# Optimization experiments

Measured on AMD Instinct MI355X. Metric: run time of the kernel, lower is better.

Reference implementation:

```python
import jax, jax.numpy as jnp
import numpy as np

NUM_HEAD = 8
GN_GROUPS = 32
EPS = 1e-5


def group_norm(x, w, b):
    # x: [B,C,H,W]; GroupNorm over 32 groups
    B, C, H, W = x.shape
    xg = x.reshape(B, GN_GROUPS, C // GN_GROUPS, H, W)
    mu = jnp.mean(xg, axis=(2, 3, 4), keepdims=True)
    var = jnp.var(xg, axis=(2, 3, 4), keepdims=True)
    xn = ((xg - mu) * jax.lax.rsqrt(var + EPS)).reshape(B, C, H, W)
    return xn * w[None, :, None, None] + b[None, :, None, None]


def conv1x1(x, w, b):
    # 1x1 conv == channel-wise linear: w [O,C], x [B,C,H,W]
    return jnp.einsum('oc,bchw->bohw', w, x) + b[None, :, None, None]


def setup_inputs() -> dict:
    key = jax.random.key(0)
    ks = jax.random.split(key, 6)
    B, C, H, W = 8, 512, 32, 32
    s = 1.0 / np.sqrt(C)
    return {
        'x': jax.random.normal(ks[0], (B, C, H, W), jnp.float32),
        'gn_w': jnp.ones((C,), jnp.float32),
        'gn_b': jnp.zeros((C,), jnp.float32),
        'wq': jax.random.normal(ks[1], (C, C), jnp.float32) * s,
        'bq': jnp.zeros((C,), jnp.float32),
        'wk': jax.random.normal(ks[2], (C, C), jnp.float32) * s,
        'bk': jnp.zeros((C,), jnp.float32),
        'wv': jax.random.normal(ks[3], (C, C), jnp.float32) * s,
        'bv': jnp.zeros((C,), jnp.float32),
        'wo': jax.random.normal(ks[4], (C, C), jnp.float32) * s,
        'bo': jnp.zeros((C,), jnp.float32),
    }


def reference(x, gn_w, gn_b, wq, bq, wk, bk, wv, bv, wo, bo):
    B, C, H, W = x.shape
    Hn = NUM_HEAD
    d = C // Hn
    N = H * W
    scale = d ** -0.5

    xn = group_norm(x, gn_w, gn_b)
    q = conv1x1(xn, wq, bq).reshape(B, Hn, d, N)  # [B,Hn,d,N]
    k = conv1x1(xn, wk, bk).reshape(B, Hn, d, N)
    v = conv1x1(xn, wv, bv).reshape(B, Hn, d, N)

    # attn[b,h,i,j] = sum_d q[b,h,d,i] * k[b,h,d,j]
    attn = jnp.einsum('bhdi,bhdj->bhij', q, k) * scale
    attn = jax.nn.softmax(attn, axis=-1)
    # out[b,h,d,i] = sum_j attn[b,h,i,j] * v[b,h,d,j]
    out = jnp.einsum('bhij,bhdj->bhdi', attn, v).reshape(B, C, H, W)
    return x + conv1x1(out, wo, bo)
```

## Files before the change

### kernel.cpp

```cpp
#include <hip/hip_runtime.h>
#include <hip/hip_bf16.h>

typedef unsigned short ushort_t;
typedef __bf16 bf16_t;
typedef bf16_t bf16x8 __attribute__((ext_vector_type(8)));
typedef float f32x4 __attribute__((ext_vector_type(4)));
typedef float f32x16 __attribute__((ext_vector_type(16)));

#define CH 512
#define NSP 1024

__device__ __forceinline__ float bf2f(ushort_t u) {
    union { unsigned int i; float f; } t; t.i = ((unsigned int)u) << 16; return t.f;
}
__device__ __forceinline__ ushort_t f2bf(float f) {
    union { float fl; unsigned int i; } t; t.fl = f;
    unsigned int r = t.i + 0x7fffu + ((t.i >> 16) & 1u);
    return (ushort_t)(r >> 16);
}
__device__ __forceinline__ unsigned int pk2(float a, float b) {
    __hip_bfloat162 h = __float22bfloat162_rn(make_float2(a, b));
    union { __hip_bfloat162 h2; unsigned int u; } t; t.h2 = h; return t.u;
}

#if __has_builtin(__builtin_amdgcn_global_load_lds)
#define HAVE_ASYNC_LDS 1
#endif
__device__ __forceinline__ void cp16(const ushort_t* g, ushort_t* l) {
#ifdef HAVE_ASYNC_LDS
    __builtin_amdgcn_global_load_lds((const __attribute__((address_space(1))) unsigned int*)g,
                                     (__attribute__((address_space(3))) unsigned int*)l, 16, 0, 0);
#else
    *(uint4*)l = *(const uint4*)g;
#endif
}

#if __has_builtin(__builtin_amdgcn_exp2f)
#define EXP2(x) __builtin_amdgcn_exp2f(x)
#else
#define EXP2(x) exp2f(x)
#endif

#define QSCALE 0.18033688011112042f

__global__ __launch_bounds__(256) void prep_gn(const float* __restrict__ x, const float* __restrict__ gw,
                                               const float* __restrict__ gbias,
                                               const float* __restrict__ w0, const float* __restrict__ w1,
                                               const float* __restrict__ w2, const float* __restrict__ w3,
                                               ushort_t* __restrict__ wbf, ushort_t* __restrict__ xnt) {
    int tid = threadIdx.x;
    if (blockIdx.x >= 256) {
        int idx = (blockIdx.x - 256) * 256 + tid;
        int my = idx >> 16;
        const float* src = (my == 0) ? w0 : (my == 1) ? w1 : (my == 2) ? w2 : w3;
        float4 v = reinterpret_cast<const float4*>(src)[idx & 65535];
        uint2 u = make_uint2(pk2(v.x, v.y), pk2(v.z, v.w));
        reinterpret_cast<uint2*>(wbf + (size_t)my * 262144)[idx & 65535] = u;
        return;
    }
    __shared__ float red[8];
    int bg = blockIdx.x;
    int b = bg >> 5, g = bg & 31;
    const float4* x4 = reinterpret_cast<const float4*>(x + (size_t)bg * 16384);
    float4 v[16];
    float s = 0.f, s2 = 0.f;
    #pragma unroll
    for (int i = 0; i < 16; i++) {
        v[i] = x4[i * 256 + tid];
        s  += v[i].x + v[i].y + v[i].z + v[i].w;
        s2 += v[i].x * v[i].x + v[i].y * v[i].y + v[i].z * v[i].z + v[i].w * v[i].w;
    }
    #pragma unroll
    for (int off = 32; off > 0; off >>= 1) {
        s  += __shfl_down(s, off, 64);
        s2 += __shfl_down(s2, off, 64);
    }
    int wv = tid >> 6;
    if ((tid & 63) == 0) { red[wv] = s; red[4 + wv] = s2; }
    __syncthreads();
    float ts  = red[0] + red[1] + red[2] + red[3];
    float ts2 = red[4] + red[5] + red[6] + red[7];
    float mu  = ts * (1.f / 16384.f);
    float var = ts2 * (1.f / 16384.f) - mu * mu;
    float rstd = rsqrtf(var + 1e-5f);
    float ca[16], cb[16];
    #pragma unroll
    for (int cc = 0; cc < 16; cc++) {
        float ww = gw[g * 16 + cc], bb = gbias[g * 16 + cc];
        ca[cc] = rstd * ww; cb[cc] = bb - mu * ca[cc];
    }
    #pragma unroll
    for (int jj = 0; jj < 4; jj++) {
        float e[16];
        #pragma unroll
        for (int cc = 0; cc < 16; cc++) {
            float xv = (jj == 0) ? v[cc].x : (jj == 1) ? v[cc].y : (jj == 2) ? v[cc].z : v[cc].w;
            e[cc] = xv * ca[cc] + cb[cc];
        }
        uint4 u0 = make_uint4(pk2(e[0], e[1]), pk2(e[2], e[3]), pk2(e[4], e[5]), pk2(e[6], e[7]));
        uint4 u1 = make_uint4(pk2(e[8], e[9]), pk2(e[10], e[11]), pk2(e[12], e[13]), pk2(e[14], e[15]));
        ushort_t* dst = xnt + ((size_t)(b * 1024 + 4 * tid + jj)) * 512 + g * 16;
        *reinterpret_cast<uint4*>(dst)     = u0;
        *reinterpret_cast<uint4*>(dst + 8) = u1;
    }
}

__global__ __launch_bounds__(256) void conv_qkv(const ushort_t* __restrict__ xnt,
                                                const ushort_t* __restrict__ wbf,
                                                const float* __restrict__ bq,
                                                const float* __restrict__ bk,
                                                const float* __restrict__ bv,
                                                ushort_t* __restrict__ qt,
                                                ushort_t* __restrict__ kt,
                                                ushort_t* __restrict__ vt) {
    __shared__ __align__(16) char smem[17408];
    ushort_t* als = (ushort_t*)smem;
    ushort_t* bls = (ushort_t*)(smem + 8192);
    int tid = threadIdx.x;
    int wave = tid >> 6, lane = tid & 63, l15 = lane & 15, quad = lane >> 4;
    int wm = wave >> 1, wn = wave & 1;
    int m0 = blockIdx.x * 128, o0 = blockIdx.y * 64, b = blockIdx.z;
    const ushort_t* A = xnt + (size_t)b * 524288;

    f32x4 acc[4][2];
    #pragma unroll
    for (int ms = 0; ms < 4; ms++)
        #pragma unroll
        for (int ns = 0; ns < 2; ns++) acc[ms][ns] = (f32x4){0.f, 0.f, 0.f, 0.f};

    for (int k0 = 0; k0 < 512; k0 += 32) {
        #pragma unroll
        for (int rep = 0; rep < 2; rep++) {
            int id = rep * 256 + tid;
            int r = id >> 2, part = id & 3;
            int sw = part ^ ((r >> 2) & 3);
            cp16(A + (size_t)(m0 + r) * 512 + k0 + sw * 8, als + (size_t)id * 8);
        }
        {
            int r = tid >> 2, part = tid & 3;
            int sw = part ^ ((r >> 2) & 3);
            cp16(wbf + (size_t)(o0 + r) * 512 + k0 + sw * 8, bls + (size_t)tid * 8);
        }
        __syncthreads();
        bf16x8 af[4], bfr[2];
        #pragma unroll
        for (int ms = 0; ms < 4; ms++) {
            int row = wm * 64 + ms * 16 + l15;
            int slot = quad ^ ((row >> 2) & 3);
            af[ms] = *(const bf16x8*)(als + row * 32 + slot * 8);
        }
        #pragma unroll
        for (int ns = 0; ns < 2; ns++) {
            int row = wn * 32 + ns * 16 + l15;
            int slot = quad ^ ((row >> 2) & 3);
            bfr[ns] = *(const bf16x8*)(bls + row * 32 + slot * 8);
        }
        #pragma unroll
        for (int ms = 0; ms < 4; ms++)
            #pragma unroll
            for (int ns = 0; ns < 2; ns++)
                acc[ms][ns] = __builtin_amdgcn_mfma_f32_16x16x32_bf16(af[ms], bfr[ns], acc[ms][ns], 0, 0, 0);
        __syncthreads();
    }

    int seg = o0 >> 9, lo = o0 & 511;
    if (seg < 2) {
        const float* bias = seg ? bk : bq;
        ushort_t* dst = seg ? kt : qt;
        float s = seg ? 1.f : QSCALE;
        float bv0 = bias[lo + wn * 32 + l15];
        float bv1 = bias[lo + wn * 32 + 16 + l15];
        ushort_t* cls = (ushort_t*)smem;
        #pragma unroll
        for (int ms = 0; ms < 4; ms++)
            #pragma unroll
            for (int ns = 0; ns < 2; ns++) {
                float bb = ns ? bv1 : bv0;
                int idx = (wm * 64 + ms * 16 + quad * 4) * 64 + wn * 32 + ns * 16 + l15;
                unsigned int ua = pk2((acc[ms][ns][0] + bb) * s, (acc[ms][ns][1] + bb) * s);
                unsigned int ub = pk2((acc[ms][ns][2] + bb) * s, (acc[ms][ns][3] + bb) * s);
                cls[idx]       = (ushort_t)(ua & 0xffff);
                cls[idx + 64]  = (ushort_t)(ua >> 16);
                cls[idx + 128] = (ushort_t)(ub & 0xffff);
                cls[idx + 192] = (ushort_t)(ub >> 16);
            }
        __syncthreads();
        int h = lo >> 6;
        size_t obase = ((size_t)(b * 8 + h) * 1024 + m0) * 64;
        #pragma unroll
        for (int rep = 0; rep < 4; rep++) {
            int id = rep * 256 + tid;
            int r = id >> 3, part = id & 7;
            *(uint4*)(dst + obase + (size_t)r * 64 + part * 8) = *(const uint4*)(cls + r * 64 + part * 8);
        }
    } else {
        float bv0 = bv[lo + wn * 32 + l15];
        float bv1 = bv[lo + wn * 32 + 16 + l15];
        ushort_t* clst = (ushort_t*)smem;
        #pragma unroll
        for (int ms = 0; ms < 4; ms++)
            #pragma unroll
            for (int ns = 0; ns < 2; ns++) {
                float bb = ns ? bv1 : bv0;
                unsigned int ua = pk2(acc[ms][ns][0] + bb, acc[ms][ns][1] + bb);
                unsigned int ub = pk2(acc[ms][ns][2] + bb, acc[ms][ns][3] + bb);
                *(uint2*)(&clst[(wn * 32 + ns * 16 + l15) * 136 + wm * 64 + ms * 16 + quad * 4]) =
                    make_uint2(ua, ub);
            }
        __syncthreads();
        #pragma unroll
        for (int rep = 0; rep < 4; rep++) {
            int id = rep * 256 + tid;
            int row = id >> 4, part = id & 15;
            *(uint4*)(vt + ((size_t)(b * 512 + lo + row) * 1024 + m0 + part * 8)) =
                *(const uint4*)(clst + row * 136 + part * 8);
        }
    }
}

#define Z16 {0.f,0.f,0.f,0.f,0.f,0.f,0.f,0.f,0.f,0.f,0.f,0.f,0.f,0.f,0.f,0.f}

#define PV_STEP(JS, P) {                                                                     \
    unsigned wA0 = pk2(P[((JS)&1)*8+0], P[((JS)&1)*8+1]);                                    \
    unsigned wA1 = pk2(P[((JS)&1)*8+2], P[((JS)&1)*8+3]);                                    \
    unsigned wB0 = pk2(P[((JS)&1)*8+4], P[((JS)&1)*8+5]);                                    \
    unsigned wB1 = pk2(P[((JS)&1)*8+6], P[((JS)&1)*8+7]);                                    \
    asm("v_permlane32_swap_b32 %0, %1" : "+v"(wA0), "+v"(wB0));                              \
    asm("v_permlane32_swap_b32 %0, %1" : "+v"(wA1), "+v"(wB1));                              \
    union { unsigned u[4]; bf16x8 v; } pa_;                                                  \
    pa_.u[0] = wA0; pa_.u[1] = wA1; pa_.u[2] = wB0; pa_.u[3] = wB1;                          \
    int phys_ = (((JS) * 2) | hi) ^ r7;                                                      \
    bf16x8 vf0 = *(const bf16x8*)(vbuf + l31 * 64 + phys_ * 8);                              \
    bf16x8 vf1 = *(const bf16x8*)(vbuf + (32 + l31) * 64 + phys_ * 8);                       \
    __builtin_amdgcn_s_setprio(1);                                                           \
    vacc0 = __builtin_amdgcn_mfma_f32_32x32x16_bf16(pa_.v, vf0, vacc0, 0, 0, 0);             \
    vacc1 = __builtin_amdgcn_mfma_f32_32x32x16_bf16(pa_.v, vf1, vacc1, 0, 0, 0);             \
    __builtin_amdgcn_s_setprio(0); }

__global__ __launch_bounds__(256) void attn_kernel(const ushort_t* __restrict__ qt,
                                                   const ushort_t* __restrict__ kt,
                                                   const ushort_t* __restrict__ vt,
                                                   ushort_t* __restrict__ ao) {
    __shared__ __align__(16) ushort_t smem[24576];
    int tid = threadIdx.x;
    int wave = tid >> 6, lane = tid & 63, l31 = lane & 31, hi = lane >> 5;
    int id = blockIdx.x;
    int bh = (id & 7) * 8 + (id >> 6);
    int i0 = ((id >> 3) & 7) * 128;
    const ushort_t* qb = qt + (size_t)bh * 65536;
    const ushort_t* kb = kt + (size_t)bh * 65536;
    const ushort_t* vb = vt + (size_t)bh * 65536;
    int iw0 = i0 + wave * 32;
    int r7 = l31 & 7;

    bf16x8 qf[4];
    #pragma unroll
    for (int ks = 0; ks < 4; ks++)
        qf[ks] = *(const bf16x8*)(qb + (size_t)(iw0 + l31) * 64 + ks * 16 + hi * 8);

    f32x16 vacc0 = Z16, vacc1 = Z16;
    float lacc = 0.f;

    int rk0 = tid >> 3, sk = tid & 7, rk1 = rk0 + 32;
    const ushort_t* kg0 = kb + rk0 * 64 + (sk ^ (rk0 & 7)) * 8;
    const ushort_t* kg1 = kb + rk1 * 64 + (sk ^ (rk1 & 7)) * 8;
    const ushort_t* vg0 = vb + (size_t)rk0 * 1024 + (sk ^ (rk0 & 7)) * 8;
    const ushort_t* vg1 = vb + (size_t)rk1 * 1024 + (sk ^ (rk1 & 7)) * 8;

    cp16(kg0, smem + tid * 8);
    cp16(kg1, smem + (tid + 256) * 8);
    cp16(vg0, smem + 12288 + tid * 8);
    cp16(vg1, smem + 12288 + (tid + 256) * 8);
    kg0 += 4096; kg1 += 4096; vg0 += 64; vg1 += 64;
    cp16(kg0, smem + 4096 + tid * 8);
    cp16(kg1, smem + 4096 + (tid + 256) * 8);
    cp16(vg0, smem + 16384 + tid * 8);
    cp16(vg1, smem + 16384 + (tid + 256) * 8);
    kg0 += 4096; kg1 += 4096; vg0 += 64; vg1 += 64;

    for (int jt = 0; jt < 16; jt++) {
        if (jt == 15) asm volatile("s_waitcnt vmcnt(0)" ::: "memory");
        else          asm volatile("s_waitcnt vmcnt(4)" ::: "memory");
        __builtin_amdgcn_s_barrier();
        __builtin_amdgcn_sched_barrier(0);
        if (jt < 14) {
            int nb = jt + 2 - ((jt + 2) >= 3 ? 3 : 0) - ((jt + 2) >= 6 ? 3 : 0)
                     - ((jt + 2) >= 9 ? 3 : 0) - ((jt + 2) >= 12 ? 3 : 0) - ((jt + 2) >= 15 ? 3 : 0);
            ushort_t* kd = smem + nb * 4096;
            ushort_t* vd = smem + 12288 + nb * 4096;
            cp16(kg0, kd + tid * 8);
            cp16(kg1, kd + (tid + 256) * 8);
            cp16(vg0, vd + tid * 8);
            cp16(vg1, vd + (tid + 256) * 8);
            kg0 += 4096; kg1 += 4096; vg0 += 64; vg1 += 64;
        }
        int cur = jt - (jt >= 3 ? 3 : 0) - (jt >= 6 ? 3 : 0) - (jt >= 9 ? 3 : 0)
                  - (jt >= 12 ? 3 : 0) - (jt >= 15 ? 3 : 0);
        const ushort_t* kbuf = smem + cur * 4096;
        const ushort_t* vbuf = smem + 12288 + cur * 4096;

        f32x16 s0 = Z16, s1 = Z16;
        __builtin_amdgcn_s_setprio(1);
        #pragma unroll
        for (int ks = 0; ks < 4; ks++) {
            int phys = ((ks * 2) | hi) ^ r7;
            bf16x8 kf = *(const bf16x8*)(kbuf + l31 * 64 + phys * 8);
            s0 = __builtin_amdgcn_mfma_f32_32x32x16_bf16(kf, qf[ks], s0, 0, 0, 0);
        }
        #pragma unroll
        for (int ks = 0; ks < 4; ks++) {
            int phys = ((ks * 2) | hi) ^ r7;
            bf16x8 kf = *(const bf16x8*)(kbuf + (32 + l31) * 64 + phys * 8);
            s1 = __builtin_amdgcn_mfma_f32_32x32x16_bf16(kf, qf[ks], s1, 0, 0, 0);
        }
        __builtin_amdgcn_s_setprio(0);

        float p0[16], p1[16];
        #pragma unroll
        for (int r = 0; r < 16; r++) p0[r] = EXP2(s0[r]);
        #pragma unroll
        for (int r = 0; r < 16; r++) p1[r] = EXP2(s1[r]);
        float t0 = 0.f, t1 = 0.f, t2 = 0.f, t3 = 0.f;
        #pragma unroll
        for (int r = 0; r < 4; r++) { t0 += p0[r]; t1 += p0[4 + r]; t2 += p0[8 + r]; t3 += p0[12 + r]; }
        #pragma unroll
        for (int r = 0; r < 4; r++) { t0 += p1[r]; t1 += p1[4 + r]; t2 += p1[8 + r]; t3 += p1[12 + r]; }
        lacc += (t0 + t1) + (t2 + t3);

        PV_STEP(0, p0)
        PV_STEP(1, p0)
        PV_STEP(2, p1)
        PV_STEP(3, p1)
    }

    __syncthreads();

    lacc += __shfl_xor(lacc, 32, 64);
    float linv[16];
    #pragma unroll
    for (int r = 0; r < 16; r++) {
        int ir = (r & 3) + 8 * (r >> 2) + 4 * hi;
        linv[r] = 1.f / __shfl(lacc, ir, 64);
    }

    ushort_t* ols = smem;
    #pragma unroll
    for (int r = 0; r < 16; r++) {
        int irow = wave * 32 + (r & 3) + 8 * (r >> 2) + 4 * hi;
        ols[irow * 80 + l31]      = f2bf(vacc0[r] * linv[r]);
        ols[irow * 80 + 32 + l31] = f2bf(vacc1[r] * linv[r]);
    }
    __syncthreads();
    int b = bh >> 3, h = bh & 7;
    ushort_t* aob = ao + ((size_t)b * 1024 + i0) * 512 + h * 64;
    #pragma unroll
    for (int rep = 0; rep < 4; rep++) {
        int idd = rep * 256 + tid;
        int rl = idd >> 3, part = idd & 7;
        *(uint4*)(aob + (size_t)rl * 512 + part * 8) = *(const uint4*)(ols + rl * 80 + part * 8);
    }
}

__global__ __launch_bounds__(256) void conv_out(const ushort_t* __restrict__ ao,
                                                const ushort_t* __restrict__ wo,
                                                const float* __restrict__ bo,
                                                const float* __restrict__ xres,
                                                float* __restrict__ out) {
    __shared__ __align__(16) char smem[12288];
    ushort_t* als = (ushort_t*)smem;
    ushort_t* bls = (ushort_t*)(smem + 8192);
    int tid = threadIdx.x;
    int wave = tid >> 6, lane = tid & 63, l15 = lane & 15, quad = lane >> 4;
    int wm = wave >> 1, wn = wave & 1;
    int m0 = blockIdx.x * 128, o0 = blockIdx.y * 64, b = blockIdx.z;
    const ushort_t* A = ao + (size_t)b * 524288;

    f32x4 acc[4][2];
    #pragma unroll
    for (int ms = 0; ms < 4; ms++)
        #pragma unroll
        for (int ns = 0; ns < 2; ns++) acc[ms][ns] = (f32x4){0.f, 0.f, 0.f, 0.f};

    for (int k0 = 0; k0 < 512; k0 += 32) {
        #pragma unroll
        for (int rep = 0; rep < 2; rep++) {
            int id = rep * 256 + tid;
            int r = id >> 2, part = id & 3;
            int sw = part ^ ((r >> 2) & 3);
            cp16(A + (size_t)(m0 + r) * 512 + k0 + sw * 8, als + (size_t)id * 8);
        }
        {
            int r = tid >> 2, part = tid & 3;
            int sw = part ^ ((r >> 2) & 3);
            cp16(wo + (size_t)(o0 + r) * 512 + k0 + sw * 8, bls + (size_t)tid * 8);
        }
        __syncthreads();
        bf16x8 af[4], bfr[2];
        #pragma unroll
        for (int ms = 0; ms < 4; ms++) {
            int row = wm * 64 + ms * 16 + l15;
            int slot = quad ^ ((row >> 2) & 3);
            af[ms] = *(const bf16x8*)(als + row * 32 + slot * 8);
        }
        #pragma unroll
        for (int ns = 0; ns < 2; ns++) {
            int row = wn * 32 + ns * 16 + l15;
            int slot = quad ^ ((row >> 2) & 3);
            bfr[ns] = *(const bf16x8*)(bls + row * 32 + slot * 8);
        }
        #pragma unroll
        for (int ms = 0; ms < 4; ms++)
            #pragma unroll
            for (int ns = 0; ns < 2; ns++)
                acc[ms][ns] = __builtin_amdgcn_mfma_f32_16x16x32_bf16(af[ms], bfr[ns], acc[ms][ns], 0, 0, 0);
        __syncthreads();
    }

    #pragma unroll
    for (int ns = 0; ns < 2; ns++) {
        int o = o0 + wn * 32 + ns * 16 + l15;
        float bb = bo[o];
        #pragma unroll
        for (int ms = 0; ms < 4; ms++) {
            int n = m0 + wm * 64 + ms * 16 + quad * 4;
            size_t ga = ((size_t)(b * 512 + o)) * 1024 + n;
            float4 xv = *(const float4*)(xres + ga);
            float4 c4;
            c4.x = acc[ms][ns][0] + bb + xv.x;
            c4.y = acc[ms][ns][1] + bb + xv.y;
            c4.z = acc[ms][ns][2] + bb + xv.z;
            c4.w = acc[ms][ns][3] + bb + xv.w;
            *(float4*)(out + ga) = c4;
        }
    }
}

extern "C" void kernel_launch(void* const* d_in, const int* in_sizes, int n_in,
                              void* d_out, int out_size, void* d_ws, size_t ws_size,
                              hipStream_t stream) {
    const float* x    = (const float*)d_in[0];
    const float* gn_w = (const float*)d_in[1];
    const float* gn_b = (const float*)d_in[2];
    const float* wq   = (const float*)d_in[3];
    const float* bq   = (const float*)d_in[4];
    const float* wk   = (const float*)d_in[5];
    const float* bk   = (const float*)d_in[6];
    const float* wv   = (const float*)d_in[7];
    const float* bv   = (const float*)d_in[8];
    const float* wo   = (const float*)d_in[9];
    const float* bo   = (const float*)d_in[10];

    char* ws = (char*)d_ws;
    ushort_t* xnt  = (ushort_t*)(ws);
    ushort_t* qt   = (ushort_t*)(ws + (((size_t)8)  << 20));
    ushort_t* kt   = (ushort_t*)(ws + (((size_t)16) << 20));
    ushort_t* vt   = (ushort_t*)(ws + (((size_t)24) << 20));
    ushort_t* wbf  = (ushort_t*)(ws + (((size_t)32) << 20));
    ushort_t* ao   = xnt;

    prep_gn<<<1280, 256, 0, stream>>>(x, gn_w, gn_b, wq, wk, wv, wo, wbf, xnt);

    conv_qkv<<<dim3(8, 24, 8), 256, 0, stream>>>(xnt, wbf, bq, bk, bv, qt, kt, vt);

    attn_kernel<<<512, 256, 0, stream>>>(qt, kt, vt, ao);

    conv_out<<<dim3(8, 8, 8), 256, 0, stream>>>(ao, wbf + 786432, bo, x, (float*)d_out);
}
```

Before: 155.3 us.

## Fuse output projection into attention kernel via per-tile spin-wait counters

Merges the attention and output 1x1 conv kernels into one launch. After writing its attention output tile, each block increments a global counter for its (batch, row-tile) group and spin-waits until all 8 heads have arrived. It then computes the 128x64 output projection tile, adding the bias and the residual. This removes one kernel launch and the tail and idle gap between the two kernels. The risk is a deadlock if all 512 blocks cannot be co-resident, plus spin-wait stalls; counters are reset in prep_gn.

Result: slower. 268.6 us (+72.9%).

```diff
diff --git a/kernel.cpp b/kernel.cpp
--- a/kernel.cpp
+++ b/kernel.cpp
@@ -43,12 +43,33 @@
 
 #define QSCALE 0.18033688011112042f
 
+#define Z16 {0.f,0.f,0.f,0.f,0.f,0.f,0.f,0.f,0.f,0.f,0.f,0.f,0.f,0.f,0.f,0.f}
+
+#define PV_STEP(JS, P) {                                                                     \
+    unsigned wA0 = pk2(P[((JS)&1)*8+0], P[((JS)&1)*8+1]);                                    \
+    unsigned wA1 = pk2(P[((JS)&1)*8+2], P[((JS)&1)*8+3]);                                    \
+    unsigned wB0 = pk2(P[((JS)&1)*8+4], P[((JS)&1)*8+5]);                                    \
+    unsigned wB1 = pk2(P[((JS)&1)*8+6], P[((JS)&1)*8+7]);                                    \
+    asm("v_permlane32_swap_b32 %0, %1" : "+v"(wA0), "+v"(wB0));                              \
+    asm("v_permlane32_swap_b32 %0, %1" : "+v"(wA1), "+v"(wB1));                              \
+    union { unsigned u[4]; bf16x8 v; } pa_;                                                  \
+    pa_.u[0] = wA0; pa_.u[1] = wA1; pa_.u[2] = wB0; pa_.u[3] = wB1;                          \
+    int phys_ = (((JS) * 2) | hi) ^ r7;                                                      \
+    bf16x8 vf0 = *(const bf16x8*)(vbuf + l31 * 64 + phys_ * 8);                              \
+    bf16x8 vf1 = *(const bf16x8*)(vbuf + (32 + l31) * 64 + phys_ * 8);                       \
+    __builtin_amdgcn_s_setprio(1);                                                           \
+    vacc0 = __builtin_amdgcn_mfma_f32_32x32x16_bf16(pa_.v, vf0, vacc0, 0, 0, 0);             \
+    vacc1 = __builtin_amdgcn_mfma_f32_32x32x16_bf16(pa_.v, vf1, vacc1, 0, 0, 0);             \
+    __builtin_amdgcn_s_setprio(0); }
+
 __global__ __launch_bounds__(256) void prep_gn(const float* __restrict__ x, const float* __restrict__ gw,
                                                const float* __restrict__ gbias,
                                                const float* __restrict__ w0, const float* __restrict__ w1,
                                                const float* __restrict__ w2, const float* __restrict__ w3,
-                                               ushort_t* __restrict__ wbf, ushort_t* __restrict__ xnt) {
+                                               ushort_t* __restrict__ wbf, ushort_t* __restrict__ xnt,
+                                               int* __restrict__ cnt) {
     int tid = threadIdx.x;
+    if (blockIdx.x == 0 && tid < 64) cnt[tid] = 0;
     if (blockIdx.x >= 256) {
         int idx = (blockIdx.x - 256) * 256 + tid;
         int my = idx >> 16;
@@ -218,29 +239,15 @@
     }
 }
 
-#define Z16 {0.f,0.f,0.f,0.f,0.f,0.f,0.f,0.f,0.f,0.f,0.f,0.f,0.f,0.f,0.f,0.f}
-
-#define PV_STEP(JS, P) {                                                                     \
-    unsigned wA0 = pk2(P[((JS)&1)*8+0], P[((JS)&1)*8+1]);                                    \
-    unsigned wA1 = pk2(P[((JS)&1)*8+2], P[((JS)&1)*8+3]);                                    \
-    unsigned wB0 = pk2(P[((JS)&1)*8+4], P[((JS)&1)*8+5]);                                    \
-    unsigned wB1 = pk2(P[((JS)&1)*8+6], P[((JS)&1)*8+7]);                                    \
-    asm("v_permlane32_swap_b32 %0, %1" : "+v"(wA0), "+v"(wB0));                              \
-    asm("v_permlane32_swap_b32 %0, %1" : "+v"(wA1), "+v"(wB1));                              \
-    union { unsigned u[4]; bf16x8 v; } pa_;                                                  \
-    pa_.u[0] = wA0; pa_.u[1] = wA1; pa_.u[2] = wB0; pa_.u[3] = wB1;                          \
-    int phys_ = (((JS) * 2) | hi) ^ r7;                                                      \
-    bf16x8 vf0 = *(const bf16x8*)(vbuf + l31 * 64 + phys_ * 8);                              \
-    bf16x8 vf1 = *(const bf16x8*)(vbuf + (32 + l31) * 64 + phys_ * 8);                       \
-    __builtin_amdgcn_s_setprio(1);                                                           \
-    vacc0 = __builtin_amdgcn_mfma_f32_32x32x16_bf16(pa_.v, vf0, vacc0, 0, 0, 0);             \
-    vacc1 = __builtin_amdgcn_mfma_f32_32x32x16_bf16(pa_.v, vf1, vacc1, 0, 0, 0);             \
-    __builtin_amdgcn_s_setprio(0); }
-
-__global__ __launch_bounds__(256) void attn_kernel(const ushort_t* __restrict__ qt,
-                                                   const ushort_t* __restrict__ kt,
-                                                   const ushort_t* __restrict__ vt,
-                                                   ushort_t* __restrict__ ao) {
+__global__ __launch_bounds__(256) void attn_out(const ushort_t* __restrict__ qt,
+                                                const ushort_t* __restrict__ kt,
+                                                const ushort_t* __restrict__ vt,
+                                                ushort_t* __restrict__ ao,
+                                                const ushort_t* __restrict__ wo,
+                                                const float* __restrict__ bo,
+                                                const float* __restrict__ xres,
+                                                float* __restrict__ out,
+                                                int* __restrict__ cnt) {
     __shared__ __align__(16) ushort_t smem[24576];
     int tid = threadIdx.x;
     int wave = tid >> 6, lane = tid & 63, l31 = lane & 31, hi = lane >> 5;
@@ -359,78 +366,84 @@
         int rl = idd >> 3, part = idd & 7;
         *(uint4*)(aob + (size_t)rl * 512 + part * 8) = *(const uint4*)(ols + rl * 80 + part * 8);
     }
-}
-
-__global__ __launch_bounds__(256) void conv_out(const ushort_t* __restrict__ ao,
-                                                const ushort_t* __restrict__ wo,
-                                                const float* __restrict__ bo,
-                                                const float* __restrict__ xres,
-                                                float* __restrict__ out) {
-    __shared__ __align__(16) char smem[12288];
-    ushort_t* als = (ushort_t*)smem;
-    ushort_t* bls = (ushort_t*)(smem + 8192);
-    int tid = threadIdx.x;
-    int wave = tid >> 6, lane = tid & 63, l15 = lane & 15, quad = lane >> 4;
-    int wm = wave >> 1, wn = wave & 1;
-    int m0 = blockIdx.x * 128, o0 = blockIdx.y * 64, b = blockIdx.z;
-    const ushort_t* A = ao + (size_t)b * 524288;
-
-    f32x4 acc[4][2];
-    #pragma unroll
-    for (int ms = 0; ms < 4; ms++)
-        #pragma unroll
-        for (int ns = 0; ns < 2; ns++) acc[ms][ns] = (f32x4){0.f, 0.f, 0.f, 0.f};
-
-    for (int k0 = 0; k0 < 512; k0 += 32) {
-        #pragma unroll
-        for (int rep = 0; rep < 2; rep++) {
-            int id = rep * 256 + tid;
-            int r = id >> 2, part = id & 3;
-            int sw = part ^ ((r >> 2) & 3);
-            cp16(A + (size_t)(m0 + r) * 512 + k0 + sw * 8, als + (size_t)id * 8);
-        }
-        {
-            int r = tid >> 2, part = tid & 3;
-            int sw = part ^ ((r >> 2) & 3);
-            cp16(wo + (size_t)(o0 + r) * 512 + k0 + sw * 8, bls + (size_t)tid * 8);
-        }
+
+    int g = b * 8 + (i0 >> 7);
+    __threadfence();
+    __syncthreads();
+    if (tid == 0) {
+        atomicAdd(&cnt[g], 1);
+        while (__hip_atomic_load(&cnt[g], __ATOMIC_ACQUIRE, __HIP_MEMORY_SCOPE_AGENT) < 8)
+            __builtin_amdgcn_s_sleep(8);
+    }
+    __syncthreads();
+    __threadfence();
+
+    {
+        int m0 = i0, o0 = h * 64;
+        ushort_t* als = smem;
+        ushort_t* bls = smem + 4096;
+        int l15 = lane & 15, quad = lane >> 4;
+        int wm = wave >> 1, wn = wave & 1;
+        const ushort_t* A = ao + (size_t)b * 524288;
+
+        f32x4 acc[4][2];
+        #pragma unroll
+        for (int ms = 0; ms < 4; ms++)
+            #pragma unroll
+            for (int ns = 0; ns < 2; ns++) acc[ms][ns] = (f32x4){0.f, 0.f, 0.f, 0.f};
+
         __syncthreads();
-        bf16x8 af[4], bfr[2];
-        #pragma unroll
-        for (int ms = 0; ms < 4; ms++) {
-            int row = wm * 64 + ms * 16 + l15;
-            int slot = quad ^ ((row >> 2) & 3);
-            af[ms] = *(const bf16x8*)(als + row * 32 + slot * 8);
-        }
+        for (int k0 = 0; k0 < 512; k0 += 32) {
+            #pragma unroll
+            for (int rep = 0; rep < 2; rep++) {
+                int idd = rep * 256 + tid;
+                int r = idd >> 2, part = idd & 3;
+                int sw = part ^ ((r >> 2) & 3);
+                cp16(A + (size_t)(m0 + r) * 512 + k0 + sw * 8, als + (size_t)idd * 8);
+            }
+            {
+                int r = tid >> 2, part = tid & 3;
+                int sw = part ^ ((r >> 2) & 3);
+                cp16(wo + (size_t)(o0 + r) * 512 + k0 + sw * 8, bls + (size_t)tid * 8);
+            }
+            __syncthreads();
+            bf16x8 af[4], bfr[2];
+            #pragma unroll
+            for (int ms = 0; ms < 4; ms++) {
+                int row = wm * 64 + ms * 16 + l15;
+                int slot = quad ^ ((row >> 2) & 3);
+                af[ms] = *(const bf16x8*)(als + row * 32 + slot * 8);
+            }
+            #pragma unroll
+            for (int ns = 0; ns < 2; ns++) {
+                int row = wn * 32 + ns * 16 + l15;
+                int slot = quad ^ ((row >> 2) & 3);
+                bfr[ns] = *(const bf16x8*)(bls + row * 32 + slot * 8);
+            }
+            #pragma unroll
+            for (int ms = 0; ms < 4; ms++)
+                #pragma unroll
+                for (int ns = 0; ns < 2; ns++)
+                    acc[ms][ns] = __builtin_amdgcn_mfma_f32_16x16x32_bf16(af[ms], bfr[ns], acc[ms][ns], 0, 0, 0);
+            __syncthreads();
+        }
+
         #pragma unroll
         for (int ns = 0; ns < 2; ns++) {
-            int row = wn * 32 + ns * 16 + l15;
-            int slot = quad ^ ((row >> 2) & 3);
-            bfr[ns] = *(const bf16x8*)(bls + row * 32 + slot * 8);
-        }
-        #pragma unroll
-        for (int ms = 0; ms < 4; ms++)
-            #pragma unroll
-            for (int ns = 0; ns < 2; ns++)
-                acc[ms][ns] = __builtin_amdgcn_mfma_f32_16x16x32_bf16(af[ms], bfr[ns], acc[ms][ns], 0, 0, 0);
-        __syncthreads();
-    }
-
-    #pragma unroll
-    for (int ns = 0; ns < 2; ns++) {
-        int o = o0 + wn * 32 + ns * 16 + l15;
-        float bb = bo[o];
-        #pragma unroll
-        for (int ms = 0; ms < 4; ms++) {
-            int n = m0 + wm * 64 + ms * 16 + quad * 4;
-            size_t ga = ((size_t)(b * 512 + o)) * 1024 + n;
-            float4 xv = *(const float4*)(xres + ga);
-            float4 c4;
-            c4.x = acc[ms][ns][0] + bb + xv.x;
-            c4.y = acc[ms][ns][1] + bb + xv.y;
-            c4.z = acc[ms][ns][2] + bb + xv.z;
-            c4.w = acc[ms][ns][3] + bb + xv.w;
-            *(float4*)(out + ga) = c4;
+            int o = o0 + wn * 32 + ns * 16 + l15;
+            float bb = bo[o];
+            #pragma unroll
+            for (int ms = 0; ms < 4; ms++) {
+                int n = m0 + wm * 64 + ms * 16 + quad * 4;
+                size_t ga = ((size_t)(b * 512 + o)) * 1024 + n;
+                float4 xv = *(const float4*)(xres + ga);
+                float4 c4;
+                c4.x = acc[ms][ns][0] + bb + xv.x;
+                c4.y = acc[ms][ns][1] + bb + xv.y;
+                c4.z = acc[ms][ns][2] + bb + xv.z;
+                c4.w = acc[ms][ns][3] + bb + xv.w;
+                *(float4*)(out + ga) = c4;
+            }
         }
     }
 }
@@ -456,13 +469,12 @@
     ushort_t* kt   = (ushort_t*)(ws + (((size_t)16) << 20));
     ushort_t* vt   = (ushort_t*)(ws + (((size_t)24) << 20));
     ushort_t* wbf  = (ushort_t*)(ws + (((size_t)32) << 20));
+    int*      cnt  = (int*)     (ws + (((size_t)35) << 20));
     ushort_t* ao   = xnt;
 
-    prep_gn<<<1280, 256, 0, stream>>>(x, gn_w, gn_b, wq, wk, wv, wo, wbf, xnt);
+    prep_gn<<<1280, 256, 0, stream>>>(x, gn_w, gn_b, wq, wk, wv, wo, wbf, xnt, cnt);
 
     conv_qkv<<<dim3(8, 24, 8), 256, 0, stream>>>(xnt, wbf, bq, bk, bv, qt, kt, vt);
 
-    attn_kernel<<<512, 256, 0, stream>>>(qt, kt, vt, ao);
-
-    conv_out<<<dim3(8, 8, 8), 256, 0, stream>>>(ao, wbf + 786432, bo, x, (float*)d_out);
-}
+    attn_out<<<512, 256, 0, stream>>>(qt, kt, vt, ao, wbf + 786432, bo, x, (float*)d_out, cnt);
+}
```
